# Kernel optimization log

Hardware: AMD Instinct MI355X
Metric: run time of the kernel (lower is better)

The kernel has to match this reference:

```python
import jax, jax.numpy as jnp
import numpy as np

CH = 512
NUM_HEADS = 8
NUM_GROUPS = 32  # min(32, channels)
EPS = 1e-5


def setup_inputs() -> dict:
    key = jax.random.key(0)
    ks = jax.random.split(key, 4)
    B, C, H, W = 8, CH, 32, 32
    x = jax.random.normal(ks[0], (B, C, H, W), dtype=jnp.float32)
    gn_weight = jnp.ones((C,), dtype=jnp.float32)
    gn_bias = jnp.zeros((C,), dtype=jnp.float32)
    # 1x1 conv weights stored as [out_ch, in_ch] (kernel dims squeezed)
    qkv_weight = jax.random.normal(ks[1], (3 * C, C), dtype=jnp.float32) * (C ** -0.5)
    qkv_bias = jnp.zeros((3 * C,), dtype=jnp.float32)
    proj_weight = jax.random.normal(ks[2], (C, C), dtype=jnp.float32) * (C ** -0.5)
    proj_bias = jnp.zeros((C,), dtype=jnp.float32)
    return {
        "x": x,
        "gn_weight": gn_weight,
        "gn_bias": gn_bias,
        "qkv_weight": qkv_weight,
        "qkv_bias": qkv_bias,
        "proj_weight": proj_weight,
        "proj_bias": proj_bias,
    }


def _group_norm(x, weight, bias):
    B, C, H, W = x.shape
    g = x.reshape(B, NUM_GROUPS, C // NUM_GROUPS, H, W)
    mean = jnp.mean(g, axis=(2, 3, 4), keepdims=True)
    var = jnp.var(g, axis=(2, 3, 4), keepdims=True)
    g = (g - mean) * jax.lax.rsqrt(var + EPS)
    g = g.reshape(B, C, H, W)
    return g * weight[None, :, None, None] + bias[None, :, None, None]


def reference(x, gn_weight, gn_bias, qkv_weight, qkv_bias, proj_weight, proj_bias):
    B, C, H, W = x.shape
    nh = NUM_HEADS
    hc = C // nh
    N = H * W

    h = _group_norm(x, gn_weight, gn_bias)
    # 1x1 conv == per-pixel matmul
    qkv = jnp.einsum('oc,bchw->bohw', qkv_weight, h) + qkv_bias[None, :, None, None]
    q, k, v = jnp.split(qkv, 3, axis=1)
    # b (h c) x y -> b h c (x y)
    q = q.reshape(B, nh, hc, N)
    k = k.reshape(B, nh, hc, N)
    v = v.reshape(B, nh, hc, N)

    scale = hc ** -0.5
    attn = jnp.einsum('bhci,bhcj->bhij', q, k) * scale  # [B, nh, N, N]
    attn = jax.nn.softmax(attn, axis=-1)
    out = jnp.einsum('bhij,bhcj->bhci', attn, v)  # [B, nh, hc, N]
    out = out.reshape(B, C, H, W)
    out = jnp.einsum('oc,bchw->bohw', proj_weight, out) + proj_bias[None, :, None, None]
    return x + out
```

## Files before the change

### kernel.cpp

```cpp
#include <hip/hip_runtime.h>
#include <math.h>

#define B_   8
#define C_   512
#define N_   1024
#define NH_  8
#define HC_  64

typedef __attribute__((ext_vector_type(8))) short bf16x8;
typedef __attribute__((ext_vector_type(4))) float f32x4;
typedef __attribute__((ext_vector_type(16))) float f32x16;

#define MFMA16(a, b, c) __builtin_amdgcn_mfma_f32_16x16x32_bf16(a, b, c, 0, 0, 0)
#define MFMA32(a, b, c) __builtin_amdgcn_mfma_f32_32x32x16_bf16(a, b, c, 0, 0, 0)

__device__ __forceinline__ unsigned short f2bf(float f) {
  unsigned u = __builtin_bit_cast(unsigned, f);
  u += 0x7fffu + ((u >> 16) & 1u);
  return (unsigned short)(u >> 16);
}

__device__ __forceinline__ unsigned short f2bf_trunc(float f) {
  return (unsigned short)(__builtin_bit_cast(unsigned, f) >> 16);
}

__device__ __forceinline__ unsigned pack2(float a, float b) {
  return (unsigned)f2bf(a) | ((unsigned)f2bf(b) << 16);
}

__device__ __forceinline__ void gll16(const void* g, void* l) {
  __builtin_amdgcn_global_load_lds(
      (const __attribute__((address_space(1))) unsigned int*)g,
      (__attribute__((address_space(3))) unsigned int*)l, 16, 0, 0);
}

__global__ __launch_bounds__(256) void prep(const float* __restrict__ x,
                                            const float* __restrict__ gw,
                                            const float* __restrict__ gb,
                                            const float* __restrict__ qkvw,
                                            const float* __restrict__ pw,
                                            unsigned short* __restrict__ hT,
                                            unsigned short* __restrict__ qkvw_bf,
                                            unsigned short* __restrict__ projw_bf) {
  const int t = threadIdx.x;
  if (blockIdx.x >= 256) {
    const int widx = blockIdx.x - 256;
    const float* src = (widx < 768) ? qkvw : pw;
    unsigned short* dst = (widx < 768) ? qkvw_bf : projw_bf;
    const int i = ((widx < 768) ? widx : widx - 768) * 1024 + t * 4;
    const float4 v = *(const float4*)(src + i);
    ushort4 o;
    o.x = f2bf(v.x); o.y = f2bf(v.y); o.z = f2bf(v.z); o.w = f2bf(v.w);
    *(ushort4*)(dst + i) = o;
    return;
  }
  const int b = blockIdx.x >> 5;
  const int g = blockIdx.x & 31;
  const float* xg = x + ((size_t)b * C_ + (size_t)g * 16) * N_;

  float4 xv[16];
  float s = 0.f, ss = 0.f;
#pragma unroll
  for (int k = 0; k < 16; ++k) {
    xv[k] = *(const float4*)(xg + (size_t)k * N_ + t * 4);
    s  += xv[k].x + xv[k].y + xv[k].z + xv[k].w;
    ss += xv[k].x * xv[k].x + xv[k].y * xv[k].y + xv[k].z * xv[k].z + xv[k].w * xv[k].w;
  }
#pragma unroll
  for (int off = 32; off > 0; off >>= 1) {
    s  += __shfl_down(s, off);
    ss += __shfl_down(ss, off);
  }
  __shared__ float rs[4], rss[4], sh_mi[2];
  if ((t & 63) == 0) { rs[t >> 6] = s; rss[t >> 6] = ss; }
  __syncthreads();
  if (t == 0) {
    s  = rs[0] + rs[1] + rs[2] + rs[3];
    ss = rss[0] + rss[1] + rss[2] + rss[3];
    const float mean = s * (1.f / 16384.f);
    const float var  = ss * (1.f / 16384.f) - mean * mean;
    sh_mi[0] = mean;
    sh_mi[1] = rsqrtf(var + 1e-5f);
  }
  __syncthreads();
  const float mean = sh_mi[0], inv = sh_mi[1];

  float sc[16], of[16];
#pragma unroll
  for (int k = 0; k < 16; ++k) {
    const int c = g * 16 + k;
    sc[k] = inv * gw[c];
    of[k] = gb[c] - mean * sc[k];
  }
#pragma unroll
  for (int r = 0; r < 4; ++r) {
    const int p = t * 4 + r;
    unsigned short* dst = hT + ((size_t)b * N_ + p) * C_ + g * 16;
    uint4 o0, o1;
#pragma unroll
    for (int k2 = 0; k2 < 4; ++k2) {
      const float a0 = ((const float*)&xv[k2 * 2 + 0])[r] * sc[k2 * 2 + 0] + of[k2 * 2 + 0];
      const float a1 = ((const float*)&xv[k2 * 2 + 1])[r] * sc[k2 * 2 + 1] + of[k2 * 2 + 1];
      ((unsigned*)&o0)[k2] = pack2(a0, a1);
      const float b0 = ((const float*)&xv[8 + k2 * 2 + 0])[r] * sc[8 + k2 * 2 + 0] + of[8 + k2 * 2 + 0];
      const float b1 = ((const float*)&xv[8 + k2 * 2 + 1])[r] * sc[8 + k2 * 2 + 1] + of[8 + k2 * 2 + 1];
      ((unsigned*)&o1)[k2] = pack2(b0, b1);
    }
    *(uint4*)(dst)     = o0;
    *(uint4*)(dst + 8) = o1;
  }
}

__global__ __launch_bounds__(256, 3) void gemm_qkv(
    const unsigned short* __restrict__ A, const float* __restrict__ bias,
    const unsigned short* __restrict__ BT, unsigned short* __restrict__ qkTout,
    unsigned short* __restrict__ vout) {
  __shared__ __attribute__((aligned(16))) short lds[128 * 136];
  const int t = threadIdx.x;
  const int lane = t & 63, w = t >> 6;
  const int lm = lane & 15, q = lane >> 4;
  const int wm = w >> 1, wn = w & 1;
  const int b = blockIdx.z;
  const int m0 = blockIdx.y * 128, n0 = blockIdx.x * 128;
  const unsigned short* Bb = BT + (size_t)b * N_ * C_;

  f32x4 acc[4][4];
#pragma unroll
  for (int i = 0; i < 4; ++i)
#pragma unroll
    for (int j = 0; j < 4; ++j) acc[i][j] = (f32x4){0.f, 0.f, 0.f, 0.f};

#define QKV_STAGE(k0, base_)                                                   \
  {                                                                            \
    _Pragma("unroll") for (int rr = 0; rr < 2; ++rr) {                         \
      const int rg = w * 2 + rr;                                               \
      gll16(A  + (size_t)(m0 + rg * 16 + lm) * C_ + (k0) + q * 8,              \
            (base_) + rg * 512);                                               \
      gll16(Bb + (size_t)(n0 + rg * 16 + lm) * C_ + (k0) + q * 8,              \
            (base_) + (8 + rg) * 512);                                         \
    }                                                                          \
  }

#define QKV_COMPUTE(base_)                                                     \
  {                                                                            \
    bf16x8 af[4];                                                              \
    _Pragma("unroll") for (int mi = 0; mi < 4; ++mi)                           \
      af[mi] = *(const bf16x8*)((base_) + (wm * 4 + mi) * 512 + lane * 8);     \
    _Pragma("unroll") for (int ni = 0; ni < 4; ++ni) {                         \
      const bf16x8 bfr =                                                       \
          *(const bf16x8*)((base_) + (8 + wn * 4 + ni) * 512 + lane * 8);      \
      _Pragma("unroll") for (int mi = 0; mi < 4; ++mi)                         \
        acc[mi][ni] = MFMA16(af[mi], bfr, acc[mi][ni]);                        \
    }                                                                          \
  }

  QKV_STAGE(0, lds)
  for (int it = 0; it < 15; ++it) {
    __syncthreads();
    short* nxt = lds + ((it + 1) & 1) * 8192;
    QKV_STAGE((it + 1) * 32, nxt)
    const short* cur = lds + (it & 1) * 8192;
    QKV_COMPUTE(cur)
  }
  __syncthreads();
  QKV_COMPUTE(lds + 8192)
#undef QKV_STAGE
#undef QKV_COMPUTE

  __syncthreads();
  if (blockIdx.y < 8) {
    const float qs = (blockIdx.y < 4) ? 0.18033688011112042f : 1.0f;
#pragma unroll
    for (int mi = 0; mi < 4; ++mi) {
#pragma unroll
      for (int ni = 0; ni < 4; ++ni) {
        const int pl = wn * 64 + ni * 16 + lm;
        const int ol0 = wm * 64 + mi * 16 + q * 4;
        ushort4 o4;
        o4.x = f2bf((acc[mi][ni][0] + bias[m0 + ol0 + 0]) * qs);
        o4.y = f2bf((acc[mi][ni][1] + bias[m0 + ol0 + 1]) * qs);
        o4.z = f2bf((acc[mi][ni][2] + bias[m0 + ol0 + 2]) * qs);
        o4.w = f2bf((acc[mi][ni][3] + bias[m0 + ol0 + 3]) * qs);
        *(ushort4*)&lds[pl * 136 + ol0] = o4;
      }
    }
    __syncthreads();
#pragma unroll
    for (int u = 0; u < 8; ++u) {
      const int flat = u * 256 + t;
      const int oc = flat & 15, pl = flat >> 4;
      *(uint4*)&qkTout[((size_t)b * N_ + n0 + pl) * 1024 + m0 + oc * 8] =
          *(const uint4*)&lds[pl * 136 + oc * 8];
    }
  } else {
#pragma unroll
    for (int mi = 0; mi < 4; ++mi)
#pragma unroll
      for (int ni = 0; ni < 4; ++ni) {
        const int pl = wn * 64 + ni * 16 + lm;
#pragma unroll
        for (int r = 0; r < 4; ++r) {
          const int ol = wm * 64 + mi * 16 + q * 4 + r;
          lds[ol * 136 + pl] = f2bf(acc[mi][ni][r] + bias[m0 + ol]);
        }
      }
    __syncthreads();
    const int c0 = m0 - 1024;
#pragma unroll
    for (int u = 0; u < 8; ++u) {
      const int flat = u * 256 + t;
      const int pc = flat & 15, ol = flat >> 4;
      *(uint4*)&vout[((size_t)b * 512 + c0 + ol) * N_ + n0 + pc * 8] =
          *(const uint4*)&lds[ol * 136 + pc * 8];
    }
  }
}

__global__ __launch_bounds__(256, 4) void gemm_proj(
    const unsigned short* __restrict__ A, const float* __restrict__ bias,
    const unsigned short* __restrict__ BT, const float* __restrict__ resid,
    float* __restrict__ outf) {
  __shared__ __attribute__((aligned(16))) short lds[32 * 512];
  const int t = threadIdx.x;
  const int lane = t & 63, w = t >> 6;
  const int lm = lane & 15, q = lane >> 4;
  const int wm = w >> 1, wn = w & 1;
  const int b = blockIdx.z;
  const int m0 = blockIdx.y * 64, n0 = blockIdx.x * 64;
  const unsigned short* Bb = BT + (size_t)b * N_ * C_;

  f32x4 acc[2][2];
#pragma unroll
  for (int i = 0; i < 2; ++i)
#pragma unroll
    for (int j = 0; j < 2; ++j) acc[i][j] = (f32x4){0.f, 0.f, 0.f, 0.f};

  for (int k0 = 0; k0 < C_; k0 += 128) {
    __syncthreads();
#pragma unroll
    for (int ks = 0; ks < 4; ++ks) {
      gll16(A  + (size_t)(m0 + w * 16 + lm) * C_ + k0 + ks * 32 + q * 8,
            lds + (w * 4 + ks) * 512);
      gll16(Bb + (size_t)(n0 + w * 16 + lm) * C_ + k0 + ks * 32 + q * 8,
            lds + (16 + w * 4 + ks) * 512);
    }
    __syncthreads();
#pragma unroll
    for (int ks = 0; ks < 4; ++ks) {
      bf16x8 af[2];
#pragma unroll
      for (int mi = 0; mi < 2; ++mi)
        af[mi] = *(const bf16x8*)(lds + ((wm * 2 + mi) * 4 + ks) * 512 + lane * 8);
#pragma unroll
      for (int ni = 0; ni < 2; ++ni) {
        const bf16x8 bfr =
            *(const bf16x8*)(lds + (16 + (wn * 2 + ni) * 4 + ks) * 512 + lane * 8);
#pragma unroll
        for (int mi = 0; mi < 2; ++mi)
          acc[mi][ni] = MFMA16(af[mi], bfr, acc[mi][ni]);
      }
    }
  }

#pragma unroll
  for (int mi = 0; mi < 2; ++mi)
#pragma unroll
    for (int ni = 0; ni < 2; ++ni) {
      const int col = n0 + wn * 32 + ni * 16 + lm;
#pragma unroll
      for (int r = 0; r < 4; ++r) {
        const int row = m0 + wm * 32 + mi * 16 + q * 4 + r;
        const size_t oi = ((size_t)b * 512 + row) * N_ + col;
        outf[oi] = acc[mi][ni][r] + bias[row] + resid[oi];
      }
    }
}

__global__ __launch_bounds__(256, 2) void attn_mfma(
    const unsigned short* __restrict__ qkT, const unsigned short* __restrict__ vbuf,
    unsigned short* __restrict__ aoT) {
  __shared__ __attribute__((aligned(16))) short lds[21504];
  short* Ks = lds;
  short* Vs = lds + 8192;
  short* Pb = lds + 12288;

  const int t = threadIdx.x;
  const int l = t & 63, w = t >> 6;
  const int l31 = l & 31, lh = l >> 5;
  const int id = blockIdx.x;
  const int xcd = id & 7, slot = id >> 3;
  const int pair = xcd * 8 + (slot >> 3);
  const int b = pair >> 3, hh = pair & 7;
  const int i0 = (slot & 7) * 128;

  const unsigned short* QT = qkT + (size_t)b * N_ * 1024;
  const unsigned short* Vp = vbuf + ((size_t)b * 512 + hh * 64) * N_;
  short* Pw = Pb + w * 2304;

  bf16x8 af[4];
#pragma unroll
  for (int kc = 0; kc < 4; ++kc)
    af[kc] = *(const bf16x8*)(QT + (size_t)(i0 + w * 32 + l31) * 1024 +
                              hh * 64 + kc * 16 + lh * 8);

  f32x16 accO[2];
#pragma unroll
  for (int r2 = 0; r2 < 16; ++r2) { accO[0][r2] = 0.f; accO[1][r2] = 0.f; }
  float lrun = 0.f;

#pragma unroll
  for (int rr = 0; rr < 2; ++rr) {
    const int idx = w * 2 + rr, jb = idx >> 2, kc = idx & 3;
    gll16(QT + (size_t)(jb * 32 + l31) * 1024 + 512 + hh * 64 + kc * 16 + lh * 8,
          Ks + idx * 512);
  }

  for (int jt = 0; jt < 16; ++jt) {
    const int j0 = jt * 64;
    __syncthreads();
#pragma unroll
    for (int rr = 0; rr < 2; ++rr) {
      const int idx = w * 2 + rr, nc = idx >> 2, kj = idx & 3;
      gll16(Vp + (size_t)(nc * 32 + l31) * N_ + j0 + kj * 16 + lh * 8,
            Vs + idx * 512);
    }
    if (jt < 15) {
#pragma unroll
      for (int rr = 0; rr < 2; ++rr) {
        const int idx = w * 2 + rr, jb = idx >> 2, kc = idx & 3;
        gll16(QT + (size_t)(j0 + 64 + jb * 32 + l31) * 1024 + 512 + hh * 64 +
                  kc * 16 + lh * 8,
              Ks + ((jt + 1) & 1) * 4096 + idx * 512);
      }
    }
    const short* Kc = Ks + (jt & 1) * 4096;

    f32x16 accS[2];
#pragma unroll
    for (int r2 = 0; r2 < 16; ++r2) { accS[0][r2] = 0.f; accS[1][r2] = 0.f; }
    __builtin_amdgcn_s_setprio(1);
#pragma unroll
    for (int kc = 0; kc < 4; ++kc)
#pragma unroll
      for (int jb = 0; jb < 2; ++jb) {
        const bf16x8 kfr = *(const bf16x8*)(Kc + (jb * 4 + kc) * 512 + l * 8);
        accS[jb] = MFMA32(kfr, af[kc], accS[jb]);
      }
    __builtin_amdgcn_s_setprio(0);

    uint4 pa4[4];
#pragma unroll
    for (int jb = 0; jb < 2; ++jb) {
      float p[16];
#pragma unroll
      for (int rg = 0; rg < 16; ++rg) {
        p[rg] = __builtin_exp2f(accS[jb][rg]);
        lrun += p[rg];
      }
      unsigned own[8];
#pragma unroll
      for (int i2 = 0; i2 < 8; ++i2)
        asm("v_cvt_pk_bf16_f32 %0, %1, %2"
            : "=v"(own[i2]) : "v"(p[2 * i2]), "v"(p[2 * i2 + 1]));
#pragma unroll
      for (int m = 0; m < 2; ++m) {
        unsigned x0 = own[4 * m + 0], y0 = own[4 * m + 2];
        unsigned x1 = own[4 * m + 1], y1 = own[4 * m + 3];
        asm("v_permlane32_swap_b32 %0, %1" : "+v"(x0), "+v"(y0));
        asm("v_permlane32_swap_b32 %0, %1" : "+v"(x1), "+v"(y1));
        pa4[jb * 2 + m] = (uint4){x0, x1, y0, y1};
      }
    }

    __syncthreads();

    __builtin_amdgcn_s_setprio(1);
#pragma unroll
    for (int kj = 0; kj < 4; ++kj) {
      const bf16x8 pf = __builtin_bit_cast(bf16x8, pa4[kj]);
#pragma unroll
      for (int nc = 0; nc < 2; ++nc) {
        const bf16x8 vf = *(const bf16x8*)(Vs + (nc * 4 + kj) * 512 + l * 8);
        accO[nc] = MFMA32(pf, vf, accO[nc]);
      }
    }
    __builtin_amdgcn_s_setprio(0);
  }

  const float lr = lrun + __shfl_xor(lrun, 32);
  float* lw = (float*)Pw;
  lw[l31] = 1.f / lr;
  float linvr[16];
#pragma unroll
  for (int rg = 0; rg < 16; ++rg)
    linvr[rg] = lw[(rg & 3) + ((rg >> 2) << 3) + (lh << 2)];

#pragma unroll
  for (int nc = 0; nc < 2; ++nc)
#pragma unroll
    for (int rg = 0; rg < 16; ++rg) {
      const int rowi = (rg & 3) + ((rg >> 2) << 3) + (lh << 2);
      Pw[rowi * 72 + nc * 32 + l31] = (short)f2bf(accO[nc][rg] * linvr[rg]);
    }
  unsigned short* aob = aoT + (size_t)b * N_ * C_;
#pragma unroll
  for (int u = 0; u < 4; ++u) {
    const int flat = u * 64 + l;
    const int c8 = flat & 7, row = flat >> 3;
    *(uint4*)&aob[(size_t)(i0 + w * 32 + row) * C_ + hh * 64 + c8 * 8] =
        *(const uint4*)&Pw[row * 72 + c8 * 8];
  }
}

extern "C" void kernel_launch(void* const* d_in, const int* in_sizes, int n_in,
                              void* d_out, int out_size, void* d_ws, size_t ws_size,
                              hipStream_t stream) {
  const float* x    = (const float*)d_in[0];
  const float* gw   = (const float*)d_in[1];
  const float* gb   = (const float*)d_in[2];
  const float* qkvw = (const float*)d_in[3];
  const float* qkvb = (const float*)d_in[4];
  const float* pw   = (const float*)d_in[5];
  const float* pb   = (const float*)d_in[6];
  float* out = (float*)d_out;

  unsigned short* hT       = (unsigned short*)d_ws;
  unsigned short* qkvw_bf  = hT + (size_t)B_ * N_ * C_;
  unsigned short* projw_bf = qkvw_bf + 1536 * 512;
  unsigned short* qkT      = projw_bf + 512 * 512;
  unsigned short* vbuf     = qkT + (size_t)B_ * N_ * 1024;
  unsigned short* aoTp     = vbuf + (size_t)B_ * 512 * N_;

  prep<<<1280, 256, 0, stream>>>(x, gw, gb, qkvw, pw, hT, qkvw_bf, projw_bf);
  gemm_qkv<<<dim3(8, 12, B_), 256, 0, stream>>>(qkvw_bf, qkvb, hT, qkT, vbuf);
  attn_mfma<<<512, 256, 0, stream>>>(qkT, vbuf, aoTp);
  gemm_proj<<<dim3(16, 8, B_), 256, 0, stream>>>(projw_bf, pb, aoTp, x, out);
}
```

Measured before the change: 163.8 us.

## Use single-wave attention blocks loading K/V fragments directly from global memory

The attention kernel changes from 4-wave blocks of 128 query rows that stage K and V tiles in LDS with barriers to 1-wave blocks of 32 query rows. Each wave loads its K and V MFMA fragments straight from global memory each 32-key step. This removes the __syncthreads calls and LDS traffic in the main loop. In exchange, K/V reuse across waves now depends on L1/L2 caching, global traffic rises, there is no explicit prefetch to hide load latency, and the grid grows to 2048 small blocks.

New measurement: 192.4 us. +17.4%, slower.

```diff
diff --git a/kernel.cpp b/kernel.cpp
--- a/kernel.cpp
+++ b/kernel.cpp
@@ -276,31 +276,27 @@
     }
 }
 
-__global__ __launch_bounds__(256, 2) void attn_mfma(
+__global__ __launch_bounds__(64, 2) void attn_mfma(
     const unsigned short* __restrict__ qkT, const unsigned short* __restrict__ vbuf,
     unsigned short* __restrict__ aoT) {
-  __shared__ __attribute__((aligned(16))) short lds[21504];
-  short* Ks = lds;
-  short* Vs = lds + 8192;
-  short* Pb = lds + 12288;
-
-  const int t = threadIdx.x;
-  const int l = t & 63, w = t >> 6;
+  __shared__ __attribute__((aligned(16))) short Pw[2304];
+  __shared__ float lsh[32];
+
+  const int l = threadIdx.x;
   const int l31 = l & 31, lh = l >> 5;
   const int id = blockIdx.x;
   const int xcd = id & 7, slot = id >> 3;
-  const int pair = xcd * 8 + (slot >> 3);
+  const int pair = xcd * 8 + (slot >> 5);
   const int b = pair >> 3, hh = pair & 7;
-  const int i0 = (slot & 7) * 128;
+  const int i0 = (slot & 31) * 32;
 
   const unsigned short* QT = qkT + (size_t)b * N_ * 1024;
   const unsigned short* Vp = vbuf + ((size_t)b * 512 + hh * 64) * N_;
-  short* Pw = Pb + w * 2304;
 
   bf16x8 af[4];
 #pragma unroll
   for (int kc = 0; kc < 4; ++kc)
-    af[kc] = *(const bf16x8*)(QT + (size_t)(i0 + w * 32 + l31) * 1024 +
+    af[kc] = *(const bf16x8*)(QT + (size_t)(i0 + l31) * 1024 +
                               hh * 64 + kc * 16 + lh * 8);
 
   f32x16 accO[2];
@@ -308,92 +304,67 @@
   for (int r2 = 0; r2 < 16; ++r2) { accO[0][r2] = 0.f; accO[1][r2] = 0.f; }
   float lrun = 0.f;
 
-#pragma unroll
-  for (int rr = 0; rr < 2; ++rr) {
-    const int idx = w * 2 + rr, jb = idx >> 2, kc = idx & 3;
-    gll16(QT + (size_t)(jb * 32 + l31) * 1024 + 512 + hh * 64 + kc * 16 + lh * 8,
-          Ks + idx * 512);
-  }
-
-  for (int jt = 0; jt < 16; ++jt) {
-    const int j0 = jt * 64;
-    __syncthreads();
-#pragma unroll
-    for (int rr = 0; rr < 2; ++rr) {
-      const int idx = w * 2 + rr, nc = idx >> 2, kj = idx & 3;
-      gll16(Vp + (size_t)(nc * 32 + l31) * N_ + j0 + kj * 16 + lh * 8,
-            Vs + idx * 512);
-    }
-    if (jt < 15) {
-#pragma unroll
-      for (int rr = 0; rr < 2; ++rr) {
-        const int idx = w * 2 + rr, jb = idx >> 2, kc = idx & 3;
-        gll16(QT + (size_t)(j0 + 64 + jb * 32 + l31) * 1024 + 512 + hh * 64 +
-                  kc * 16 + lh * 8,
-              Ks + ((jt + 1) & 1) * 4096 + idx * 512);
-      }
-    }
-    const short* Kc = Ks + (jt & 1) * 4096;
-
-    f32x16 accS[2];
-#pragma unroll
-    for (int r2 = 0; r2 < 16; ++r2) { accS[0][r2] = 0.f; accS[1][r2] = 0.f; }
-    __builtin_amdgcn_s_setprio(1);
+  const unsigned short* kg = QT + (size_t)l31 * 1024 + 512 + hh * 64 + lh * 8;
+  const unsigned short* vg0 = Vp + (size_t)l31 * N_ + lh * 8;
+  const unsigned short* vg1 = Vp + (size_t)(32 + l31) * N_ + lh * 8;
+
+  for (int jt = 0; jt < 32; ++jt) {
+    const int j0 = jt * 32;
+
+    bf16x8 kfr[4];
 #pragma unroll
     for (int kc = 0; kc < 4; ++kc)
-#pragma unroll
-      for (int jb = 0; jb < 2; ++jb) {
-        const bf16x8 kfr = *(const bf16x8*)(Kc + (jb * 4 + kc) * 512 + l * 8);
-        accS[jb] = MFMA32(kfr, af[kc], accS[jb]);
-      }
-    __builtin_amdgcn_s_setprio(0);
-
-    uint4 pa4[4];
-#pragma unroll
-    for (int jb = 0; jb < 2; ++jb) {
-      float p[16];
-#pragma unroll
-      for (int rg = 0; rg < 16; ++rg) {
-        p[rg] = __builtin_exp2f(accS[jb][rg]);
-        lrun += p[rg];
-      }
-      unsigned own[8];
-#pragma unroll
-      for (int i2 = 0; i2 < 8; ++i2)
-        asm("v_cvt_pk_bf16_f32 %0, %1, %2"
-            : "=v"(own[i2]) : "v"(p[2 * i2]), "v"(p[2 * i2 + 1]));
-#pragma unroll
-      for (int m = 0; m < 2; ++m) {
-        unsigned x0 = own[4 * m + 0], y0 = own[4 * m + 2];
-        unsigned x1 = own[4 * m + 1], y1 = own[4 * m + 3];
-        asm("v_permlane32_swap_b32 %0, %1" : "+v"(x0), "+v"(y0));
-        asm("v_permlane32_swap_b32 %0, %1" : "+v"(x1), "+v"(y1));
-        pa4[jb * 2 + m] = (uint4){x0, x1, y0, y1};
-      }
-    }
-
-    __syncthreads();
-
-    __builtin_amdgcn_s_setprio(1);
-#pragma unroll
-    for (int kj = 0; kj < 4; ++kj) {
+      kfr[kc] = *(const bf16x8*)(kg + (size_t)j0 * 1024 + kc * 16);
+    bf16x8 vfr[4];
+#pragma unroll
+    for (int kj = 0; kj < 2; ++kj) {
+      vfr[0 * 2 + kj] = *(const bf16x8*)(vg0 + j0 + kj * 16);
+      vfr[1 * 2 + kj] = *(const bf16x8*)(vg1 + j0 + kj * 16);
+    }
+
+    f32x16 accS;
+#pragma unroll
+    for (int r2 = 0; r2 < 16; ++r2) accS[r2] = 0.f;
+#pragma unroll
+    for (int kc = 0; kc < 4; ++kc)
+      accS = MFMA32(kfr[kc], af[kc], accS);
+
+#pragma unroll
+    for (int rg = 0; rg < 16; ++rg) {
+      const float p = __builtin_exp2f(accS[rg]);
+      accS[rg] = p;
+      lrun += p;
+    }
+    unsigned own[8];
+#pragma unroll
+    for (int i2 = 0; i2 < 8; ++i2)
+      asm("v_cvt_pk_bf16_f32 %0, %1, %2"
+          : "=v"(own[i2]) : "v"(accS[2 * i2]), "v"(accS[2 * i2 + 1]));
+    uint4 pa4[2];
+#pragma unroll
+    for (int m = 0; m < 2; ++m) {
+      unsigned x0 = own[4 * m + 0], y0 = own[4 * m + 2];
+      unsigned x1 = own[4 * m + 1], y1 = own[4 * m + 3];
+      asm("v_permlane32_swap_b32 %0, %1" : "+v"(x0), "+v"(y0));
+      asm("v_permlane32_swap_b32 %0, %1" : "+v"(x1), "+v"(y1));
+      pa4[m] = (uint4){x0, x1, y0, y1};
+    }
+
+#pragma unroll
+    for (int kj = 0; kj < 2; ++kj) {
       const bf16x8 pf = __builtin_bit_cast(bf16x8, pa4[kj]);
 #pragma unroll
-      for (int nc = 0; nc < 2; ++nc) {
-        const bf16x8 vf = *(const bf16x8*)(Vs + (nc * 4 + kj) * 512 + l * 8);
-        accO[nc] = MFMA32(pf, vf, accO[nc]);
-      }
-    }
-    __builtin_amdgcn_s_setprio(0);
+      for (int nc = 0; nc < 2; ++nc)
+        accO[nc] = MFMA32(pf, vfr[nc * 2 + kj], accO[nc]);
+    }
   }
 
   const float lr = lrun + __shfl_xor(lrun, 32);
-  float* lw = (float*)Pw;
-  lw[l31] = 1.f / lr;
+  lsh[l31] = 1.f / lr;
   float linvr[16];
 #pragma unroll
   for (int rg = 0; rg < 16; ++rg)
-    linvr[rg] = lw[(rg & 3) + ((rg >> 2) << 3) + (lh << 2)];
+    linvr[rg] = lsh[(rg & 3) + ((rg >> 2) << 3) + (lh << 2)];
 
 #pragma unroll
   for (int nc = 0; nc < 2; ++nc)
@@ -407,7 +378,7 @@
   for (int u = 0; u < 4; ++u) {
     const int flat = u * 64 + l;
     const int c8 = flat & 7, row = flat >> 3;
-    *(uint4*)&aob[(size_t)(i0 + w * 32 + row) * C_ + hh * 64 + c8 * 8] =
+    *(uint4*)&aob[(size_t)(i0 + row) * C_ + hh * 64 + c8 * 8] =
         *(const uint4*)&Pw[row * 72 + c8 * 8];
   }
 }
@@ -433,6 +404,6 @@
 
   prep<<<1280, 256, 0, stream>>>(x, gw, gb, qkvw, pw, hT, qkvw_bf, projw_bf);
   gemm_qkv<<<dim3(8, 12, B_), 256, 0, stream>>>(qkvw_bf, qkvb, hT, qkT, vbuf);
-  attn_mfma<<<512, 256, 0, stream>>>(qkT, vbuf, aoTp);
+  attn_mfma<<<2048, 64, 0, stream>>>(qkT, vbuf, aoTp);
   gemm_proj<<<dim3(16, 8, B_), 256, 0, stream>>>(projw_bf, pb, aoTp, x, out);
 }
```

## Store K and V in MFMA fragment-ordered layout for contiguous attention loads

Applied to the files above, without the earlier changes.

The QKV GEMM epilogue now writes K and V into per-(batch, head) buffers already arranged in the exact fragment order that the attention kernel copies into LDS. The attention kernel's global-to-LDS loads then read contiguous 1 KB chunks instead of strided rows, which improves coalescing and reduces address arithmetic. The cost is more complex index math in the GEMM epilogue and extra workspace, and K is no longer written to the qkT buffer.

Measured after the change: 161.5 us. Within noise of the previous version (-1.4%).

```diff
diff --git a/kernel.cpp b/kernel.cpp
--- a/kernel.cpp
+++ b/kernel.cpp
@@ -18,10 +18,6 @@
   unsigned u = __builtin_bit_cast(unsigned, f);
   u += 0x7fffu + ((u >> 16) & 1u);
   return (unsigned short)(u >> 16);
-}
-
-__device__ __forceinline__ unsigned short f2bf_trunc(float f) {
-  return (unsigned short)(__builtin_bit_cast(unsigned, f) >> 16);
 }
 
 __device__ __forceinline__ unsigned pack2(float a, float b) {
@@ -114,7 +110,7 @@
 __global__ __launch_bounds__(256, 3) void gemm_qkv(
     const unsigned short* __restrict__ A, const float* __restrict__ bias,
     const unsigned short* __restrict__ BT, unsigned short* __restrict__ qkTout,
-    unsigned short* __restrict__ vout) {
+    unsigned short* __restrict__ kfrag, unsigned short* __restrict__ vfrag) {
   __shared__ __attribute__((aligned(16))) short lds[128 * 136];
   const int t = threadIdx.x;
   const int lane = t & 63, w = t >> 6;
@@ -185,12 +181,26 @@
       }
     }
     __syncthreads();
-#pragma unroll
-    for (int u = 0; u < 8; ++u) {
-      const int flat = u * 256 + t;
-      const int oc = flat & 15, pl = flat >> 4;
-      *(uint4*)&qkTout[((size_t)b * N_ + n0 + pl) * 1024 + m0 + oc * 8] =
-          *(const uint4*)&lds[pl * 136 + oc * 8];
+    if (blockIdx.y < 4) {
+#pragma unroll
+      for (int u = 0; u < 8; ++u) {
+        const int flat = u * 256 + t;
+        const int oc = flat & 15, pl = flat >> 4;
+        *(uint4*)&qkTout[((size_t)b * N_ + n0 + pl) * 1024 + m0 + oc * 8] =
+            *(const uint4*)&lds[pl * 136 + oc * 8];
+      }
+    } else {
+      const int hh0 = (blockIdx.y - 4) * 2;
+#pragma unroll
+      for (int u = 0; u < 8; ++u) {
+        const int flat = u * 256 + t;
+        const int ll = flat & 63, kc = (flat >> 6) & 3;
+        const int jbl = (flat >> 8) & 3, hhl = flat >> 10;
+        *(uint4*)&kfrag[((((size_t)b * 8 + hh0 + hhl) * 32 + (n0 >> 5) + jbl) * 4 +
+                         kc) * 512 + ll * 8] =
+            *(const uint4*)&lds[(jbl * 32 + (ll & 31)) * 136 + hhl * 64 +
+                                kc * 16 + (ll >> 5) * 8];
+      }
     }
   } else {
 #pragma unroll
@@ -205,13 +215,16 @@
         }
       }
     __syncthreads();
-    const int c0 = m0 - 1024;
+    const int hh0 = (blockIdx.y - 8) * 2;
 #pragma unroll
     for (int u = 0; u < 8; ++u) {
       const int flat = u * 256 + t;
-      const int pc = flat & 15, ol = flat >> 4;
-      *(uint4*)&vout[((size_t)b * 512 + c0 + ol) * N_ + n0 + pc * 8] =
-          *(const uint4*)&lds[ol * 136 + pc * 8];
+      const int ll = flat & 63, kj = (flat >> 6) & 3;
+      const int jtl = (flat >> 8) & 1, nc = (flat >> 9) & 1, hhl = flat >> 10;
+      *(uint4*)&vfrag[(((((size_t)b * 8 + hh0 + hhl) * 16 + (n0 >> 6) + jtl) * 2 +
+                        nc) * 4 + kj) * 512 + ll * 8] =
+          *(const uint4*)&lds[(hhl * 64 + nc * 32 + (ll & 31)) * 136 +
+                              jtl * 64 + kj * 16 + (ll >> 5) * 8];
     }
   }
 }
@@ -277,8 +290,8 @@
 }
 
 __global__ __launch_bounds__(256, 2) void attn_mfma(
-    const unsigned short* __restrict__ qkT, const unsigned short* __restrict__ vbuf,
-    unsigned short* __restrict__ aoT) {
+    const unsigned short* __restrict__ qkT, const unsigned short* __restrict__ kfrag,
+    const unsigned short* __restrict__ vfrag, unsigned short* __restrict__ aoT) {
   __shared__ __attribute__((aligned(16))) short lds[21504];
   short* Ks = lds;
   short* Vs = lds + 8192;
@@ -294,7 +307,8 @@
   const int i0 = (slot & 7) * 128;
 
   const unsigned short* QT = qkT + (size_t)b * N_ * 1024;
-  const unsigned short* Vp = vbuf + ((size_t)b * 512 + hh * 64) * N_;
+  const unsigned short* kb = kfrag + (size_t)(b * 8 + hh) * 65536;
+  const unsigned short* vb = vfrag + (size_t)(b * 8 + hh) * 65536;
   short* Pw = Pb + w * 2304;
 
   bf16x8 af[4];
@@ -310,26 +324,22 @@
 
 #pragma unroll
   for (int rr = 0; rr < 2; ++rr) {
-    const int idx = w * 2 + rr, jb = idx >> 2, kc = idx & 3;
-    gll16(QT + (size_t)(jb * 32 + l31) * 1024 + 512 + hh * 64 + kc * 16 + lh * 8,
-          Ks + idx * 512);
+    const int idx = w * 2 + rr;
+    gll16(kb + (size_t)idx * 512 + l * 8, Ks + idx * 512);
   }
 
   for (int jt = 0; jt < 16; ++jt) {
-    const int j0 = jt * 64;
     __syncthreads();
 #pragma unroll
     for (int rr = 0; rr < 2; ++rr) {
-      const int idx = w * 2 + rr, nc = idx >> 2, kj = idx & 3;
-      gll16(Vp + (size_t)(nc * 32 + l31) * N_ + j0 + kj * 16 + lh * 8,
-            Vs + idx * 512);
+      const int idx = w * 2 + rr;
+      gll16(vb + ((size_t)jt * 8 + idx) * 512 + l * 8, Vs + idx * 512);
     }
     if (jt < 15) {
 #pragma unroll
       for (int rr = 0; rr < 2; ++rr) {
-        const int idx = w * 2 + rr, jb = idx >> 2, kc = idx & 3;
-        gll16(QT + (size_t)(j0 + 64 + jb * 32 + l31) * 1024 + 512 + hh * 64 +
-                  kc * 16 + lh * 8,
+        const int idx = w * 2 + rr;
+        gll16(kb + ((size_t)(jt + 1) * 8 + idx) * 512 + l * 8,
               Ks + ((jt + 1) & 1) * 4096 + idx * 512);
       }
     }
@@ -428,11 +438,12 @@
   unsigned short* qkvw_bf  = hT + (size_t)B_ * N_ * C_;
   unsigned short* projw_bf = qkvw_bf + 1536 * 512;
   unsigned short* qkT      = projw_bf + 512 * 512;
-  unsigned short* vbuf     = qkT + (size_t)B_ * N_ * 1024;
-  unsigned short* aoTp     = vbuf + (size_t)B_ * 512 * N_;
+  unsigned short* aoTp     = qkT + (size_t)B_ * N_ * 1024;
+  unsigned short* kfrag    = aoTp + (size_t)B_ * N_ * C_;
+  unsigned short* vfrag    = kfrag + (size_t)64 * 65536;
 
   prep<<<1280, 256, 0, stream>>>(x, gw, gb, qkvw, pw, hT, qkvw_bf, projw_bf);
-  gemm_qkv<<<dim3(8, 12, B_), 256, 0, stream>>>(qkvw_bf, qkvb, hT, qkT, vbuf);
-  attn_mfma<<<512, 256, 0, stream>>>(qkT, vbuf, aoTp);
+  gemm_qkv<<<dim3(8, 12, B_), 256, 0, stream>>>(qkvw_bf, qkvb, hT, qkT, kfrag, vfrag);
+  attn_mfma<<<512, 256, 0, stream>>>(qkT, kfrag, vfrag, aoTp);
   gemm_proj<<<dim3(16, 8, B_), 256, 0, stream>>>(projw_bf, pb, aoTp, x, out);
 }
```
